# Kernel optimization log

Hardware: AMD Instinct MI355X
Metric: run time of the kernel (lower is better)

The kernel has to match this reference:

```python
import jax, jax.numpy as jnp
import numpy as np

HEAD_COUNT = 6  # module scales by head_count**-0.5, not head_size
SCALE = HEAD_COUNT ** (-0.5)


def setup_inputs() -> dict:
    key = jax.random.key(0)
    kx, kq, kk, kv = jax.random.split(key, 4)
    B, T, C, H = 512, 128, 384, 64
    x = jax.random.normal(kx, (B, T, C), dtype=jnp.float32)
    init = (1.0 / np.sqrt(C)).astype(np.float32)
    Wq = jax.random.normal(kq, (C, H), dtype=jnp.float32) * init
    Wk = jax.random.normal(kk, (C, H), dtype=jnp.float32) * init
    Wv = jax.random.normal(kv, (C, H), dtype=jnp.float32) * init
    return {"x": x, "Wq": Wq, "Wk": Wk, "Wv": Wv}


def reference(x, Wq, Wk, Wv):
    # x: [B, T, C]; Wq/Wk/Wv: [C, H]
    q = jnp.einsum('btc,ch->bth', x, Wq)
    k = jnp.einsum('btc,ch->bth', x, Wk)
    v = jnp.einsum('btc,ch->bth', x, Wv)
    # scores: [B, T, T], scaled by head_count**-0.5 (faithful to source)
    scores = jnp.einsum('bth,bsh->bts', q, k) * SCALE
    T = x.shape[1]
    causal = jnp.tril(jnp.ones((T, T), dtype=bool))
    scores = jnp.where(causal, scores, -jnp.inf)
    weights = jax.nn.softmax(scores, axis=-1)
    # dropout omitted (eval mode / identity for reference baseline)
    return jnp.einsum('bts,bsh->bth', weights, v)
```

## Files before the change

### kernel.cpp

```cpp
#include <hip/hip_runtime.h>
#include <hip/hip_bf16.h>


#define B_ 512
#define T_ 128
#define C_ 384
#define H_ 64

typedef __bf16 bf16;
typedef __attribute__((ext_vector_type(8))) __bf16 bf16x8;
typedef __attribute__((ext_vector_type(4))) __bf16 bf16x4;
typedef __attribute__((ext_vector_type(4))) float f32x4;

#define GLOAD_LDS16(g, l)                                                     \
    __builtin_amdgcn_global_load_lds(                                         \
        (const __attribute__((address_space(1))) void*)(g),                   \
        (__attribute__((address_space(3))) void*)(l), 16, 0, 0)

__global__ void build_wt(const float* __restrict__ Wq, const float* __restrict__ Wk,
                         const float* __restrict__ Wv, bf16* __restrict__ Wt)
{
    int t = blockIdx.x * 256 + threadIdx.x;
    if (t >= 12 * 12 * 64) return;
    int lane = t & 63;
    int tn   = (t >> 6) % 12;
    int kc   = t / (12 * 64);
    int lm = lane & 15, quad = lane >> 4;
    int n = tn * 16 + lm;
    int j = n >> 6, h = n & 63;
    const float* Wp = (j == 0) ? Wq : (j == 1) ? Wk : Wv;
    int k0 = kc * 32 + quad * 8;
    bf16x8 v;
#pragma unroll
    for (int e = 0; e < 8; ++e) v[e] = (bf16)Wp[(k0 + e) * H_ + h];
    *(bf16x8*)&Wt[t * 8] = v;
}


__launch_bounds__(512, 4)
__global__ void head_fused(const float* __restrict__ x,
                           const bf16* __restrict__ Wt,
                           float* __restrict__ out)
{
    __shared__ __align__(16) bf16 lds[24576];
    bf16* Qs  = lds;
    bf16* Ks  = lds + 8192;
    bf16* Vts = lds + 16384;
    bf16* Ps  = lds;
    float* xstage = (float*)lds;

    const int tid  = threadIdx.x;
    const int w    = tid >> 6;
    const int lane = tid & 63;
    const int lm   = lane & 15;
    const int quad = lane >> 4;
    const int mg   = w >> 2;
    const int ng   = w & 3;
    const int b    = blockIdx.x;

    const float* xb = x + (size_t)b * (T_ * C_);

    f32x4 acc[4][3];
#pragma unroll
    for (int mf = 0; mf < 4; ++mf)
#pragma unroll
        for (int nf = 0; nf < 3; ++nf) acc[mf][nf] = (f32x4){0.f, 0.f, 0.f, 0.f};

    const bf16* wbase = Wt + (size_t)(3 * ng) * 512 + lane * 8;

    const int u0row = tid >> 3, u0unit = tid & 7;
    const int u1row = (tid + 512) >> 3, u1unit = tid & 7;
    const float* g0 = xb + (size_t)u0row * C_ + (u0unit ^ (u0row & 7)) * 4;
    const float* g1 = xb + (size_t)u1row * C_ + (u1unit ^ (u1row & 7)) * 4;
    char* l0 = (char*)lds + (size_t)(w * 64) * 16;
    char* l1 = (char*)lds + (size_t)(512 + w * 64) * 16;

    auto STAGE = [&](int kc) {
        int bo = (kc % 3) * 16384;
        GLOAD_LDS16(g0 + kc * 32, l0 + bo);
        GLOAD_LDS16(g1 + kc * 32, l1 + bo);
    };

    STAGE(0);
    STAGE(1);
    asm volatile("s_waitcnt vmcnt(2)" ::: "memory");
    __builtin_amdgcn_s_barrier();

#pragma unroll
    for (int kc = 0; kc < 12; ++kc) {
        if (kc + 2 < 12) STAGE(kc + 2);

        const float* xc = xstage + (kc % 3) * 4096;
        bf16x8 afr[4];
#pragma unroll
        for (int mf = 0; mf < 4; ++mf) {
            int row = 64 * mg + 16 * mf + lm;
            int p0 = (2 * quad) ^ (row & 7);
            int p1 = (2 * quad + 1) ^ (row & 7);
            f32x4 va = *(const f32x4*)(xc + row * 32 + p0 * 4);
            f32x4 vb = *(const f32x4*)(xc + row * 32 + p1 * 4);
            afr[mf] = (bf16x8){(bf16)va[0], (bf16)va[1], (bf16)va[2], (bf16)va[3],
                               (bf16)vb[0], (bf16)vb[1], (bf16)vb[2], (bf16)vb[3]};
        }
#pragma unroll
        for (int nf = 0; nf < 3; ++nf) {
            bf16x8 bfr = *(const bf16x8*)(wbase + (size_t)kc * 6144 + nf * 512);
#pragma unroll
            for (int mf = 0; mf < 4; ++mf)
                acc[mf][nf] =
                    __builtin_amdgcn_mfma_f32_16x16x32_bf16(afr[mf], bfr, acc[mf][nf], 0, 0, 0);
        }

        if (kc < 11) {
            if (kc < 10) asm volatile("s_waitcnt vmcnt(2)" ::: "memory");
            else         asm volatile("s_waitcnt vmcnt(0)" ::: "memory");
            __builtin_amdgcn_s_barrier();
        }
    }
    __syncthreads();

#pragma unroll
    for (int mf = 0; mf < 4; ++mf) {
#pragma unroll
        for (int nf = 0; nf < 3; ++nf) {
            int tn = 3 * ng + nf;
            int gn = 16 * tn + lm;
            int j = gn >> 6, h = gn & 63;
            int m0 = 64 * mg + 16 * mf + quad * 4;
            if (j == 2) {
                bf16x4 v4 = {(bf16)acc[mf][nf][0], (bf16)acc[mf][nf][1],
                             (bf16)acc[mf][nf][2], (bf16)acc[mf][nf][3]};
                int pc = (m0 & 7) | ((((m0 >> 3) ^ (h & 15)) & 15) << 3);
                *(bf16x4*)&Vts[h * 128 + pc] = v4;
            } else {
                bf16* dst = (j == 0) ? Qs : Ks;
#pragma unroll
                for (int r = 0; r < 4; ++r) {
                    int m = m0 + r;
                    int pc = (h & 7) | ((((h >> 3) ^ (m & 7)) & 7) << 3);
                    dst[m * 64 + pc] = (bf16)acc[mf][nf][r];
                }
            }
        }
    }
    __syncthreads();

    const float SCALE = 0.40824829046386307f;
    const int tm = w;
    const int mrow = 16 * tm + lm;

    f32x4 sacc[8];
#pragma unroll
    for (int t = 0; t < 8; ++t) sacc[t] = (f32x4){0.f, 0.f, 0.f, 0.f};

    bf16x8 qa[2];
#pragma unroll
    for (int ks = 0; ks < 2; ++ks) {
        int phys = ((ks * 4 + quad) ^ (mrow & 7)) & 7;
        qa[ks] = *(const bf16x8*)&Qs[mrow * 64 + phys * 8];
    }
#pragma unroll
    for (int tn = 0; tn < 8; ++tn) {
        if (tn <= tm) {
            int nrow = 16 * tn + lm;
#pragma unroll
            for (int ks = 0; ks < 2; ++ks) {
                int phys = ((ks * 4 + quad) ^ (nrow & 7)) & 7;
                bf16x8 kb = *(const bf16x8*)&Ks[nrow * 64 + phys * 8];
                sacc[tn] =
                    __builtin_amdgcn_mfma_f32_16x16x32_bf16(qa[ks], kb, sacc[tn], 0, 0, 0);
            }
        }
    }

#pragma unroll
    for (int r = 0; r < 4; ++r) {
        int m = 16 * tm + quad * 4 + r;
        float mx = -1e30f;
#pragma unroll
        for (int tn = 0; tn < 8; ++tn) {
            if (tn <= tm) {
                int n = 16 * tn + lm;
                float v = (n <= m) ? sacc[tn][r] * SCALE : -1e30f;
                sacc[tn][r] = v;
                mx = fmaxf(mx, v);
            }
        }
#pragma unroll
        for (int off = 1; off < 16; off <<= 1) mx = fmaxf(mx, __shfl_xor(mx, off, 16));
        float sum = 0.f;
#pragma unroll
        for (int tn = 0; tn < 8; ++tn) {
            if (tn <= tm) {
                float e = __expf(sacc[tn][r] - mx);
                sacc[tn][r] = e;
                sum += e;
            }
        }
#pragma unroll
        for (int off = 1; off < 16; off <<= 1) sum += __shfl_xor(sum, off, 16);
        float inv = 1.f / sum;
#pragma unroll
        for (int tn = 0; tn < 8; ++tn) {
            if (tn <= tm) sacc[tn][r] *= inv;
        }
    }

    __syncthreads();

#pragma unroll
    for (int tn = 0; tn < 8; ++tn) {
        if (tn <= tm) {
            int n = 16 * tn + lm;
#pragma unroll
            for (int r = 0; r < 4; ++r) {
                int m = 16 * tm + quad * 4 + r;
                int pc = (n & 7) | ((((n >> 3) ^ (m & 15)) & 15) << 3);
                Ps[m * 128 + pc] = (bf16)sacc[tn][r];
            }
        }
    }
    if ((tm & 1) == 0) {
        int m = 16 * tm + lm;
        int c0 = 16 * (tm + 1) + quad * 4;
        int pc = (c0 & 7) | ((((c0 >> 3) ^ (m & 15)) & 15) << 3);
        *(bf16x4*)&Ps[m * 128 + pc] =
            (bf16x4){(bf16)0.f, (bf16)0.f, (bf16)0.f, (bf16)0.f};
    }

    f32x4 oacc[4];
#pragma unroll
    for (int t = 0; t < 4; ++t) oacc[t] = (f32x4){0.f, 0.f, 0.f, 0.f};

    const int nks = (tm + 2) >> 1;
    for (int ks = 0; ks < nks; ++ks) {
        int unit = ks * 4 + quad;
        int phys = (unit ^ (mrow & 15)) & 15;
        bf16x8 pa = *(const bf16x8*)&Ps[mrow * 128 + phys * 8];
#pragma unroll
        for (int th = 0; th < 4; ++th) {
            int hrow = 16 * th + lm;
            int ph2 = (unit ^ (hrow & 15)) & 15;
            bf16x8 vb = *(const bf16x8*)&Vts[hrow * 128 + ph2 * 8];
            oacc[th] =
                __builtin_amdgcn_mfma_f32_16x16x32_bf16(pa, vb, oacc[th], 0, 0, 0);
        }
    }

    float* ob = out + (size_t)b * (T_ * H_);
#pragma unroll
    for (int th = 0; th < 4; ++th) {
        int h = 16 * th + lm;
#pragma unroll
        for (int r = 0; r < 4; ++r) {
            int m = 16 * tm + quad * 4 + r;
            ob[m * 64 + h] = oacc[th][r];
        }
    }
}

extern "C" void kernel_launch(void* const* d_in, const int* in_sizes, int n_in,
                              void* d_out, int out_size, void* d_ws, size_t ws_size,
                              hipStream_t stream) {
    const float* x  = (const float*)d_in[0];
    const float* Wq = (const float*)d_in[1];
    const float* Wk = (const float*)d_in[2];
    const float* Wv = (const float*)d_in[3];
    float* o = (float*)d_out;
    bf16* Wt = (bf16*)d_ws;
    build_wt<<<dim3(36), dim3(256), 0, stream>>>(Wq, Wk, Wv, Wt);
    head_fused<<<dim3(B_), dim3(512), 0, stream>>>(x, Wt, o);
}
```

Measured before the change: 171.1 us.

## Stage weight tiles through LDS with double-buffered async loads alongside x

Weight B-fragments for the QKV projection are now copied into shared memory with global_load_lds together with the x tile, instead of each wave reading them directly from global memory. The pipeline drops from three x buffers with prefetch distance two to two combined x+W buffers with distance one, and every iteration now waits for all loads to finish. This is meant to cut redundant global/L2 traffic for the weights across waves. In exchange LDS grows from 48KB to 56KB, which may reduce occupancy, and the shallower prefetch exposes more load latency.

```diff
diff --git a/kernel.cpp b/kernel.cpp
--- a/kernel.cpp
+++ b/kernel.cpp
@@ -42,12 +42,11 @@
                            const bf16* __restrict__ Wt,
                            float* __restrict__ out)
 {
-    __shared__ __align__(16) bf16 lds[24576];
+    __shared__ __align__(16) bf16 lds[28672];
     bf16* Qs  = lds;
     bf16* Ks  = lds + 8192;
     bf16* Vts = lds + 16384;
     bf16* Ps  = lds;
-    float* xstage = (float*)lds;
 
     const int tid  = threadIdx.x;
     const int w    = tid >> 6;
@@ -66,31 +65,35 @@
 #pragma unroll
         for (int nf = 0; nf < 3; ++nf) acc[mf][nf] = (f32x4){0.f, 0.f, 0.f, 0.f};
 
-    const bf16* wbase = Wt + (size_t)(3 * ng) * 512 + lane * 8;
-
-    const int u0row = tid >> 3, u0unit = tid & 7;
-    const int u1row = (tid + 512) >> 3, u1unit = tid & 7;
-    const float* g0 = xb + (size_t)u0row * C_ + (u0unit ^ (u0row & 7)) * 4;
-    const float* g1 = xb + (size_t)u1row * C_ + (u1unit ^ (u1row & 7)) * 4;
-    char* l0 = (char*)lds + (size_t)(w * 64) * 16;
-    char* l1 = (char*)lds + (size_t)(512 + w * 64) * 16;
+    const int r0 = tid >> 3, r1 = (tid + 512) >> 3;
+    const float* gx0 = xb + (size_t)r0 * C_ + (((tid & 7) ^ (r0 & 7)) * 4);
+    const float* gx1 = xb + (size_t)r1 * C_ + (((tid & 7) ^ (r1 & 7)) * 4);
+    char* lx0 = (char*)lds + w * 1024;
+    char* lx1 = (char*)lds + 8192 + w * 1024;
+    const char* gwt = (const char*)Wt;
+    char* lw0 = (char*)lds + 16384 + w * 1024;
+    char* lw1 = (char*)lds + 16384 + 8192 + w * 1024;
 
     auto STAGE = [&](int kc) {
-        int bo = (kc % 3) * 16384;
-        GLOAD_LDS16(g0 + kc * 32, l0 + bo);
-        GLOAD_LDS16(g1 + kc * 32, l1 + bo);
+        int bo = (kc & 1) * 28672;
+        GLOAD_LDS16(gx0 + kc * 32, lx0 + bo);
+        GLOAD_LDS16(gx1 + kc * 32, lx1 + bo);
+        GLOAD_LDS16(gwt + (size_t)kc * 12288 + tid * 16, lw0 + bo);
+        if (w < 4)
+            GLOAD_LDS16(gwt + (size_t)kc * 12288 + 8192 + tid * 16, lw1 + bo);
     };
 
     STAGE(0);
-    STAGE(1);
-    asm volatile("s_waitcnt vmcnt(2)" ::: "memory");
+    asm volatile("s_waitcnt vmcnt(0)" ::: "memory");
     __builtin_amdgcn_s_barrier();
 
 #pragma unroll
     for (int kc = 0; kc < 12; ++kc) {
-        if (kc + 2 < 12) STAGE(kc + 2);
-
-        const float* xc = xstage + (kc % 3) * 4096;
+        if (kc < 11) STAGE(kc + 1);
+
+        const float* xc = (const float*)((const char*)lds + (kc & 1) * 28672);
+        const bf16*  wc = (const bf16*)((const char*)lds + (kc & 1) * 28672 + 16384);
+
         bf16x8 afr[4];
 #pragma unroll
         for (int mf = 0; mf < 4; ++mf) {
@@ -104,7 +107,7 @@
         }
 #pragma unroll
         for (int nf = 0; nf < 3; ++nf) {
-            bf16x8 bfr = *(const bf16x8*)(wbase + (size_t)kc * 6144 + nf * 512);
+            bf16x8 bfr = *(const bf16x8*)(wc + (3 * ng + nf) * 512 + lane * 8);
 #pragma unroll
             for (int mf = 0; mf < 4; ++mf)
                 acc[mf][nf] =
@@ -112,8 +115,7 @@
         }
 
         if (kc < 11) {
-            if (kc < 10) asm volatile("s_waitcnt vmcnt(2)" ::: "memory");
-            else         asm volatile("s_waitcnt vmcnt(0)" ::: "memory");
+            asm volatile("s_waitcnt vmcnt(0)" ::: "memory");
             __builtin_amdgcn_s_barrier();
         }
     }
```

New measurement: 168.2 us. Within noise of the previous version (-1.7%).
